# Kernel tuning notes

Hardware: AMD Instinct MI355X
Metric: run time of the kernel (lower is better)

Reference implementation:

```python
import jax, jax.numpy as jnp
import numpy as np

C_IN = 768
CA = 384


def dwconv3d(x, w, b, pad):
    # x: [B, Ca, T, H, W], w: [Ca, 1, kd, kh, kw] depthwise (groups=Ca)
    y = jax.lax.conv_general_dilated(
        x, w, window_strides=(1, 1, 1), padding=pad,
        dimension_numbers=("NCDHW", "OIDHW", "NCDHW"),
        feature_group_count=w.shape[0])
    return y + b[None, :, None, None, None]


def setup_inputs() -> dict:
    key = jax.random.key(0)
    ks = jax.random.split(key, 9)
    s = 0.02
    inp = {
        "x": jax.random.normal(ks[0], (128, 197, C_IN), dtype=jnp.float32),
        # main branch params (torch Linear weight transposed to [in, out])
        "w1": jax.random.normal(ks[1], (C_IN, CA), dtype=jnp.float32) * s,
        "b1": jnp.zeros((CA,), jnp.float32),
        "cw": jax.random.normal(ks[2], (CA, 1, 3, 3, 3), dtype=jnp.float32) * s,
        "cb": jnp.zeros((CA,), jnp.float32),
        "w2": jax.random.normal(ks[3], (CA, C_IN), dtype=jnp.float32) * s,
        "b2": jnp.zeros((C_IN,), jnp.float32),
        # offset-adapter params (depthwise kernel (1,3,3))
        "ow1": jax.random.normal(ks[4], (C_IN, CA), dtype=jnp.float32) * s,
        "ob1": jnp.zeros((CA,), jnp.float32),
        "ocw": jax.random.normal(ks[5], (CA, 1, 1, 3, 3), dtype=jnp.float32) * s,
        "ocb": jnp.zeros((CA,), jnp.float32),
        "ow2": jax.random.normal(ks[6], (CA, C_IN), dtype=jnp.float32) * s,
        "ob2": jnp.zeros((C_IN,), jnp.float32),
        "T": 8,
    }
    return inp


def reference(x, w1, b1, cw, cb, w2, b2, ow1, ob1, ocw, ocb, ow2, ob2, T):
    BT, L, C = x.shape
    B = BT // T
    H = W = int(round((L - 1) ** 0.5))
    Ca = w1.shape[1]

    xs = x[:, 1:, :].reshape(B, T, H * W, C)  # drop CLS token

    # ---- OffsetAdapter branch ----
    x_former = jnp.concatenate([xs[:, :1], xs[:, :-1]], axis=1)  # former_id = [0,0,1,...,T-2]
    off = xs - x_former
    off = off @ ow1 + ob1                                   # [B,T,HW,Ca]
    off = off.reshape(B, T, H, W, Ca).transpose(0, 4, 1, 2, 3)  # [B,Ca,T,H,W]
    off = dwconv3d(off, ocw, ocb, [(0, 0), (1, 1), (1, 1)])
    off = off.transpose(0, 2, 3, 4, 1).reshape(BT, H * W, Ca)
    off = off @ ow2 + ob2                                   # [BT,HW,C]

    # ---- main branch ----
    y = xs @ w1 + b1                                        # [B,T,HW,Ca]
    y = y.reshape(B, T, H, W, Ca).transpose(0, 4, 1, 2, 3)  # [B,Ca,T,H,W]
    y = dwconv3d(y, cw, cb, [(1, 1), (1, 1), (1, 1)])
    y = y.transpose(0, 2, 3, 4, 1).reshape(BT, H * W, Ca)
    y = y @ w2 + b2 + off                                   # [BT,HW,C]

    # residual add into patch tokens (CLS passthrough)
    return x.at[:, 1:, :].add(y)
```

## Files before the change

kernel.cpp:

```cpp
#include <hip/hip_runtime.h>

#define Cc   768
#define CAc  384
#define Bc   16
#define Tc   8
#define Hc   14
#define Wc   14
#define HWc  196
#define Lc   197
#define BTc  128
#define Mc   25088

typedef unsigned short u16;
typedef __attribute__((ext_vector_type(4))) float f32x4;
typedef __attribute__((ext_vector_type(4))) short s16x4;
typedef __attribute__((ext_vector_type(8))) short s16x8;

__device__ __forceinline__ u16 f2b(float f) {
  union { float f; unsigned u; } v; v.f = f;
  unsigned r = (v.u + 0x7FFFu + ((v.u >> 16) & 1u)) >> 16;
  return (u16)r;
}
__device__ __forceinline__ float b2f(u16 h) {
  union { unsigned u; float f; } v; v.u = ((unsigned)h) << 16;
  return v.f;
}

__global__ void wt_kernel(const float* __restrict__ w, u16* __restrict__ wT, int K, int N) {
  int idx = blockIdx.x * 256 + threadIdx.x;
  if (idx >= K * N) return;
  int n = idx / K, k = idx - n * K;
  wT[idx] = f2b(w[k * N + n]);
}

__global__ void cwt_kernel(const float* __restrict__ cw, float* __restrict__ cwT, int taps) {
  int idx = blockIdx.x * 256 + threadIdx.x;
  if (idx >= taps * CAc) return;
  int t = idx / CAc, c = idx - t * CAc;
  cwT[idx] = cw[c * taps + t];
}

__global__ void prep_kernel(const float* __restrict__ x, u16* __restrict__ xb, u16* __restrict__ db) {
  int idx = blockIdx.x * 256 + threadIdx.x;
  if (idx >= Mc * 96) return;
  int r = idx / 96;
  int cg = idx - r * 96;
  int b = r / (Tc * HWc);
  int rem = r - b * (Tc * HWc);
  int t = rem / HWc;
  int hw = rem - t * HWc;
  long xoff = ((long)(b * Tc + t) * Lc + 1 + hw) * Cc + cg * 8;
  long poff = (t > 0) ? (xoff - (long)Lc * Cc) : xoff;
  f32x4 ca = *(const f32x4*)(x + xoff);
  f32x4 cb = *(const f32x4*)(x + xoff + 4);
  f32x4 pa = *(const f32x4*)(x + poff);
  f32x4 pb = *(const f32x4*)(x + poff + 4);
  s16x8 xo, dd;
  #pragma unroll
  for (int q = 0; q < 4; ++q) {
    xo[q]     = (short)f2b(ca[q]);
    xo[q + 4] = (short)f2b(cb[q]);
    dd[q]     = (short)f2b(ca[q] - pa[q]);
    dd[q + 4] = (short)f2b(cb[q] - pb[q]);
  }
  *(s16x8*)(xb + (long)r * Cc + cg * 8) = xo;
  *(s16x8*)(db + (long)r * Cc + cg * 8) = dd;
}

__global__ void cls_kernel(const float* __restrict__ x, float* __restrict__ out) {
  int idx = blockIdx.x * 256 + threadIdx.x;
  if (idx >= BTc * (Cc / 4)) return;
  int bt = idx / (Cc / 4);
  int c4 = (idx - bt * (Cc / 4)) * 4;
  long o = (long)bt * Lc * Cc + c4;
  *(f32x4*)(out + o) = *(const f32x4*)(x + o);
}

#define SP 68

__global__ __launch_bounds__(256, 2) void gemm1_kernel(
    const u16* __restrict__ xb, const u16* __restrict__ db,
    const u16* __restrict__ w1T, const u16* __restrict__ ow1T,
    const float* __restrict__ b1v, const float* __restrict__ ob1v,
    u16* __restrict__ y1, u16* __restrict__ o1)
{
  __shared__ u16 lA[128 * SP];
  __shared__ u16 lB[128 * SP];
  const u16* A    = blockIdx.z ? db   : xb;
  const u16* Wt   = blockIdx.z ? ow1T : w1T;
  const float* bv = blockIdx.z ? ob1v : b1v;
  u16* outp       = blockIdx.z ? o1   : y1;

  int tid = threadIdx.x;
  int m0 = blockIdx.x * 128;
  int n0 = blockIdx.y * 128;
  int wave = tid >> 6, lane = tid & 63;
  int wm = (wave >> 1) * 64, wn = (wave & 1) * 64;
  int lrow = lane & 15, lgrp = lane >> 4;
  int srow = tid >> 3;
  int scol = (tid & 7) * 8;

  f32x4 acc[4][4];
  #pragma unroll
  for (int i = 0; i < 4; ++i)
    #pragma unroll
    for (int j = 0; j < 4; ++j) acc[i][j] = (f32x4){0.f, 0.f, 0.f, 0.f};

  for (int kt = 0; kt < 12; ++kt) {
    int k0 = kt * 64;
    #pragma unroll
    for (int p = 0; p < 4; ++p) {
      int r = p * 32 + srow;
      s16x8 va = *(const s16x8*)(A  + (long)(m0 + r) * Cc + k0 + scol);
      s16x8 vb = *(const s16x8*)(Wt + (long)(n0 + r) * Cc + k0 + scol);
      *(s16x4*)(lA + r * SP + scol)     = ((s16x4*)&va)[0];
      *(s16x4*)(lA + r * SP + scol + 4) = ((s16x4*)&va)[1];
      *(s16x4*)(lB + r * SP + scol)     = ((s16x4*)&vb)[0];
      *(s16x4*)(lB + r * SP + scol + 4) = ((s16x4*)&vb)[1];
    }
    __syncthreads();
    #pragma unroll
    for (int kk = 0; kk < 4; ++kk) {
      s16x4 af[4], bf[4];
      #pragma unroll
      for (int i = 0; i < 4; ++i) af[i] = *(const s16x4*)(lA + (wm + i * 16 + lrow) * SP + kk * 16 + lgrp * 4);
      #pragma unroll
      for (int j = 0; j < 4; ++j) bf[j] = *(const s16x4*)(lB + (wn + j * 16 + lrow) * SP + kk * 16 + lgrp * 4);
      #pragma unroll
      for (int i = 0; i < 4; ++i)
        #pragma unroll
        for (int j = 0; j < 4; ++j)
          acc[i][j] = __builtin_amdgcn_mfma_f32_16x16x16bf16_1k(af[i], bf[j], acc[i][j], 0, 0, 0);
    }
    __syncthreads();
  }
  #pragma unroll
  for (int i = 0; i < 4; ++i) {
    #pragma unroll
    for (int j = 0; j < 4; ++j) {
      int n = n0 + wn + j * 16 + lrow;
      float bb = bv[n];
      #pragma unroll
      for (int q = 0; q < 4; ++q) {
        int m = m0 + wm + i * 16 + lgrp * 4 + q;
        outp[(long)m * CAc + n] = f2b(acc[i][j][q] + bb);
      }
    }
  }
}

__global__ __launch_bounds__(256, 2) void gemm2_kernel(
    const u16* __restrict__ c1, const u16* __restrict__ c2,
    const u16* __restrict__ w2T, const u16* __restrict__ ow2T,
    const float* __restrict__ b2v, const float* __restrict__ ob2v,
    const float* __restrict__ x, float* __restrict__ out)
{
  __shared__ u16 lA[128 * SP];
  __shared__ u16 lB[128 * SP];
  int tid = threadIdx.x;
  int m0 = blockIdx.x * 128;
  int n0 = blockIdx.y * 128;
  int wave = tid >> 6, lane = tid & 63;
  int wm = (wave >> 1) * 64, wn = (wave & 1) * 64;
  int lrow = lane & 15, lgrp = lane >> 4;
  int srow = tid >> 3;
  int scol = (tid & 7) * 8;

  f32x4 acc[4][4];
  #pragma unroll
  for (int i = 0; i < 4; ++i)
    #pragma unroll
    for (int j = 0; j < 4; ++j) acc[i][j] = (f32x4){0.f, 0.f, 0.f, 0.f};

  for (int kt = 0; kt < 12; ++kt) {
    int half = kt >= 6;
    const u16* Ap = half ? c2 : c1;
    const u16* Wp = half ? ow2T : w2T;
    int k0 = (half ? (kt - 6) : kt) * 64;
    #pragma unroll
    for (int p = 0; p < 4; ++p) {
      int r = p * 32 + srow;
      s16x8 va = *(const s16x8*)(Ap + (long)(m0 + r) * CAc + k0 + scol);
      s16x8 vb = *(const s16x8*)(Wp + (long)(n0 + r) * CAc + k0 + scol);
      *(s16x4*)(lA + r * SP + scol)     = ((s16x4*)&va)[0];
      *(s16x4*)(lA + r * SP + scol + 4) = ((s16x4*)&va)[1];
      *(s16x4*)(lB + r * SP + scol)     = ((s16x4*)&vb)[0];
      *(s16x4*)(lB + r * SP + scol + 4) = ((s16x4*)&vb)[1];
    }
    __syncthreads();
    #pragma unroll
    for (int kk = 0; kk < 4; ++kk) {
      s16x4 af[4], bf[4];
      #pragma unroll
      for (int i = 0; i < 4; ++i) af[i] = *(const s16x4*)(lA + (wm + i * 16 + lrow) * SP + kk * 16 + lgrp * 4);
      #pragma unroll
      for (int j = 0; j < 4; ++j) bf[j] = *(const s16x4*)(lB + (wn + j * 16 + lrow) * SP + kk * 16 + lgrp * 4);
      #pragma unroll
      for (int i = 0; i < 4; ++i)
        #pragma unroll
        for (int j = 0; j < 4; ++j)
          acc[i][j] = __builtin_amdgcn_mfma_f32_16x16x16bf16_1k(af[i], bf[j], acc[i][j], 0, 0, 0);
    }
    __syncthreads();
  }
  #pragma unroll
  for (int i = 0; i < 4; ++i) {
    #pragma unroll
    for (int q = 0; q < 4; ++q) {
      int m = m0 + wm + i * 16 + lgrp * 4 + q;
      int bt = m / HWc;
      int hw = m - bt * HWc;
      long base = ((long)bt * Lc + 1 + hw) * Cc;
      #pragma unroll
      for (int j = 0; j < 4; ++j) {
        int n = n0 + wn + j * 16 + lrow;
        out[base + n] = x[base + n] + acc[i][j][q] + b2v[n] + ob2v[n];
      }
    }
  }
}

__global__ void conv_kernel(const u16* __restrict__ in, const float* __restrict__ wT,
                            const float* __restrict__ bias, u16* __restrict__ outp,
                            int is3d)
{
  int bth = blockIdx.x;
  int h = bth % Hc;
  int bt = bth / Hc;
  int t = bt % Tc;
  int tid = threadIdx.x;
  int dtlo = is3d ? -1 : 0, dthi = is3d ? 1 : 0;
  for (int it = tid; it < Wc * 48; it += 256) {
    int wq = it / 48;
    int c = (it - wq * 48) * 8;
    float a[8] = {0.f, 0.f, 0.f, 0.f, 0.f, 0.f, 0.f, 0.f};
    int tap = 0;
    for (int dt = dtlo; dt <= dthi; ++dt) {
      int tt = t + dt;
      bool tok = (tt >= 0) && (tt < Tc);
      for (int dh = -1; dh <= 1; ++dh) {
        int hh = h + dh;
        bool hok = (hh >= 0) && (hh < Hc);
        for (int dw = -1; dw <= 1; ++dw, ++tap) {
          int ww = wq + dw;
          if (!tok || !hok || ww < 0 || ww >= Wc) continue;
          const u16* ip = in + ((long)(bt + dt) * HWc + hh * Wc + ww) * CAc + c;
          s16x8 v = *(const s16x8*)ip;
          const float* wp = wT + tap * CAc + c;
          f32x4 w0 = *(const f32x4*)wp;
          f32x4 w1 = *(const f32x4*)(wp + 4);
          #pragma unroll
          for (int q = 0; q < 4; ++q) {
            a[q]     += b2f((u16)v[q])     * w0[q];
            a[q + 4] += b2f((u16)v[q + 4]) * w1[q];
          }
        }
      }
    }
    s16x8 o;
    #pragma unroll
    for (int q = 0; q < 8; ++q) o[q] = (short)f2b(a[q] + bias[c + q]);
    *(s16x8*)(outp + ((long)bt * HWc + h * Wc + wq) * CAc + c) = o;
  }
}

extern "C" void kernel_launch(void* const* d_in, const int* in_sizes, int n_in,
                              void* d_out, int out_size, void* d_ws, size_t ws_size,
                              hipStream_t stream) {
  const float* x   = (const float*)d_in[0];
  const float* w1  = (const float*)d_in[1];
  const float* b1  = (const float*)d_in[2];
  const float* cw  = (const float*)d_in[3];
  const float* cb  = (const float*)d_in[4];
  const float* w2  = (const float*)d_in[5];
  const float* b2  = (const float*)d_in[6];
  const float* ow1 = (const float*)d_in[7];
  const float* ob1 = (const float*)d_in[8];
  const float* ocw = (const float*)d_in[9];
  const float* ocb = (const float*)d_in[10];
  const float* ow2 = (const float*)d_in[11];
  const float* ob2 = (const float*)d_in[12];
  float* out = (float*)d_out;
  char* ws = (char*)d_ws;

  u16*  w1T  = (u16*) (ws + 0);
  u16*  ow1T = (u16*) (ws + 589824);
  u16*  w2T  = (u16*) (ws + 1179648);
  u16*  ow2T = (u16*) (ws + 1769472);
  float* cwT = (float*)(ws + 2359296);
  float* ocwT= (float*)(ws + 2400768);
  u16*  xb   = (u16*) (ws + 2414592);
  u16*  db   = (u16*) (ws + 40949760);
  u16*  y1   = (u16*) (ws + 79484928);
  u16*  o1   = (u16*) (ws + 98752512);
  u16*  c1   = (u16*) (ws + 2414592);
  u16*  c2   = (u16*) (ws + 2414592 + 19267584);

  wt_kernel<<<1152, 256, 0, stream>>>(w1, w1T, 768, 384);
  wt_kernel<<<1152, 256, 0, stream>>>(ow1, ow1T, 768, 384);
  wt_kernel<<<1152, 256, 0, stream>>>(w2, w2T, 384, 768);
  wt_kernel<<<1152, 256, 0, stream>>>(ow2, ow2T, 384, 768);
  cwt_kernel<<<41, 256, 0, stream>>>(cw, cwT, 27);
  cwt_kernel<<<14, 256, 0, stream>>>(ocw, ocwT, 9);
  prep_kernel<<<9408, 256, 0, stream>>>(x, xb, db);
  cls_kernel<<<96, 256, 0, stream>>>(x, out);
  gemm1_kernel<<<dim3(196, 3, 2), 256, 0, stream>>>(xb, db, w1T, ow1T, b1, ob1, y1, o1);
  conv_kernel<<<1792, 256, 0, stream>>>(y1, cwT, cb, c1, 1);
  conv_kernel<<<1792, 256, 0, stream>>>(o1, ocwT, ocb, c2, 0);
  gemm2_kernel<<<dim3(196, 6, 1), 256, 0, stream>>>(c1, c2, w2T, ow2T, b2, ob2, x, out);
}
```

Before: 372.1 us.

## Use 16x16x32 bf16 MFMA, wider LDS ops, tiled weight transpose, merged launches

Both GEMMs switch from the 16x16x16 bf16 MFMA to the 16x16x32 variant, with 8-element LDS reads and writes and the LDS row pitch changed from 68 to 72. Launch bounds are raised to 4 blocks per CU. Weight transposes now go through a shared-memory tile and are merged into two launches, and the two depthwise convolutions are merged into one launch. This cuts instruction count, LDS traffic and launch overhead, at the cost of more register pressure from the higher occupancy target.

```diff
diff --git a/kernel.cpp b/kernel.cpp
--- a/kernel.cpp
+++ b/kernel.cpp
@@ -2,7 +2,6 @@
 
 #define Cc   768
 #define CAc  384
-#define Bc   16
 #define Tc   8
 #define Hc   14
 #define Wc   14
@@ -26,11 +25,25 @@
   return v.f;
 }
 
-__global__ void wt_kernel(const float* __restrict__ w, u16* __restrict__ wT, int K, int N) {
-  int idx = blockIdx.x * 256 + threadIdx.x;
-  if (idx >= K * N) return;
-  int n = idx / K, k = idx - n * K;
-  wT[idx] = f2b(w[k * N + n]);
+__global__ void wt_kernel(const float* __restrict__ wA, u16* __restrict__ wAT,
+                          const float* __restrict__ wB, u16* __restrict__ wBT,
+                          int K, int N) {
+  __shared__ float t[32][33];
+  const float* w = blockIdx.z ? wB : wA;
+  u16* wT = blockIdx.z ? wBT : wAT;
+  int k0 = blockIdx.x * 32, n0 = blockIdx.y * 32;
+  int tx = threadIdx.x & 31, ty = threadIdx.x >> 5;
+  #pragma unroll
+  for (int p = 0; p < 4; ++p) {
+    int r = ty + p * 8;
+    t[r][tx] = w[(long)(k0 + r) * N + n0 + tx];
+  }
+  __syncthreads();
+  #pragma unroll
+  for (int p = 0; p < 4; ++p) {
+    int r = ty + p * 8;
+    wT[(long)(n0 + r) * K + k0 + tx] = f2b(t[tx][r]);
+  }
 }
 
 __global__ void cwt_kernel(const float* __restrict__ cw, float* __restrict__ cwT, int taps) {
@@ -76,9 +89,9 @@
   *(f32x4*)(out + o) = *(const f32x4*)(x + o);
 }
 
-#define SP 68
-
-__global__ __launch_bounds__(256, 2) void gemm1_kernel(
+#define SP 72
+
+__global__ __launch_bounds__(256, 4) void gemm1_kernel(
     const u16* __restrict__ xb, const u16* __restrict__ db,
     const u16* __restrict__ w1T, const u16* __restrict__ ow1T,
     const float* __restrict__ b1v, const float* __restrict__ ob1v,
@@ -104,7 +117,7 @@
   #pragma unroll
   for (int i = 0; i < 4; ++i)
     #pragma unroll
-    for (int j = 0; j < 4; ++j) acc[i][j] = (f32x4){0.f, 0.f, 0.f, 0.f};
+    for (int j = 0; j < 4; ++j) acc[i][j] = (f32x4){0,0,0,0};
 
   for (int kt = 0; kt < 12; ++kt) {
     int k0 = kt * 64;
@@ -113,24 +126,22 @@
       int r = p * 32 + srow;
       s16x8 va = *(const s16x8*)(A  + (long)(m0 + r) * Cc + k0 + scol);
       s16x8 vb = *(const s16x8*)(Wt + (long)(n0 + r) * Cc + k0 + scol);
-      *(s16x4*)(lA + r * SP + scol)     = ((s16x4*)&va)[0];
-      *(s16x4*)(lA + r * SP + scol + 4) = ((s16x4*)&va)[1];
-      *(s16x4*)(lB + r * SP + scol)     = ((s16x4*)&vb)[0];
-      *(s16x4*)(lB + r * SP + scol + 4) = ((s16x4*)&vb)[1];
+      *(s16x8*)(lA + r * SP + scol) = va;
+      *(s16x8*)(lB + r * SP + scol) = vb;
     }
     __syncthreads();
     #pragma unroll
-    for (int kk = 0; kk < 4; ++kk) {
-      s16x4 af[4], bf[4];
-      #pragma unroll
-      for (int i = 0; i < 4; ++i) af[i] = *(const s16x4*)(lA + (wm + i * 16 + lrow) * SP + kk * 16 + lgrp * 4);
-      #pragma unroll
-      for (int j = 0; j < 4; ++j) bf[j] = *(const s16x4*)(lB + (wn + j * 16 + lrow) * SP + kk * 16 + lgrp * 4);
+    for (int kk = 0; kk < 2; ++kk) {
+      s16x8 af[4], bf[4];
+      #pragma unroll
+      for (int i = 0; i < 4; ++i) af[i] = *(const s16x8*)(lA + (wm + i * 16 + lrow) * SP + kk * 32 + lgrp * 8);
+      #pragma unroll
+      for (int j = 0; j < 4; ++j) bf[j] = *(const s16x8*)(lB + (wn + j * 16 + lrow) * SP + kk * 32 + lgrp * 8);
       #pragma unroll
       for (int i = 0; i < 4; ++i)
         #pragma unroll
         for (int j = 0; j < 4; ++j)
-          acc[i][j] = __builtin_amdgcn_mfma_f32_16x16x16bf16_1k(af[i], bf[j], acc[i][j], 0, 0, 0);
+          acc[i][j] = __builtin_amdgcn_mfma_f32_16x16x32_bf16(af[i], bf[j], acc[i][j], 0, 0, 0);
     }
     __syncthreads();
   }
@@ -149,7 +160,7 @@
   }
 }
 
-__global__ __launch_bounds__(256, 2) void gemm2_kernel(
+__global__ __launch_bounds__(256, 4) void gemm2_kernel(
     const u16* __restrict__ c1, const u16* __restrict__ c2,
     const u16* __restrict__ w2T, const u16* __restrict__ ow2T,
     const float* __restrict__ b2v, const float* __restrict__ ob2v,
@@ -170,7 +181,7 @@
   #pragma unroll
   for (int i = 0; i < 4; ++i)
     #pragma unroll
-    for (int j = 0; j < 4; ++j) acc[i][j] = (f32x4){0.f, 0.f, 0.f, 0.f};
+    for (int j = 0; j < 4; ++j) acc[i][j] = (f32x4){0,0,0,0};
 
   for (int kt = 0; kt < 12; ++kt) {
     int half = kt >= 6;
@@ -182,24 +193,22 @@
       int r = p * 32 + srow;
       s16x8 va = *(const s16x8*)(Ap + (long)(m0 + r) * CAc + k0 + scol);
       s16x8 vb = *(const s16x8*)(Wp + (long)(n0 + r) * CAc + k0 + scol);
-      *(s16x4*)(lA + r * SP + scol)     = ((s16x4*)&va)[0];
-      *(s16x4*)(lA + r * SP + scol + 4) = ((s16x4*)&va)[1];
-      *(s16x4*)(lB + r * SP + scol)     = ((s16x4*)&vb)[0];
-      *(s16x4*)(lB + r * SP + scol + 4) = ((s16x4*)&vb)[1];
+      *(s16x8*)(lA + r * SP + scol) = va;
+      *(s16x8*)(lB + r * SP + scol) = vb;
     }
     __syncthreads();
     #pragma unroll
-    for (int kk = 0; kk < 4; ++kk) {
-      s16x4 af[4], bf[4];
-      #pragma unroll
-      for (int i = 0; i < 4; ++i) af[i] = *(const s16x4*)(lA + (wm + i * 16 + lrow) * SP + kk * 16 + lgrp * 4);
-      #pragma unroll
-      for (int j = 0; j < 4; ++j) bf[j] = *(const s16x4*)(lB + (wn + j * 16 + lrow) * SP + kk * 16 + lgrp * 4);
+    for (int kk = 0; kk < 2; ++kk) {
+      s16x8 af[4], bf[4];
+      #pragma unroll
+      for (int i = 0; i < 4; ++i) af[i] = *(const s16x8*)(lA + (wm + i * 16 + lrow) * SP + kk * 32 + lgrp * 8);
+      #pragma unroll
+      for (int j = 0; j < 4; ++j) bf[j] = *(const s16x8*)(lB + (wn + j * 16 + lrow) * SP + kk * 32 + lgrp * 8);
       #pragma unroll
       for (int i = 0; i < 4; ++i)
         #pragma unroll
         for (int j = 0; j < 4; ++j)
-          acc[i][j] = __builtin_amdgcn_mfma_f32_16x16x16bf16_1k(af[i], bf[j], acc[i][j], 0, 0, 0);
+          acc[i][j] = __builtin_amdgcn_mfma_f32_16x16x32_bf16(af[i], bf[j], acc[i][j], 0, 0, 0);
     }
     __syncthreads();
   }
@@ -220,10 +229,17 @@
   }
 }
 
-__global__ void conv_kernel(const u16* __restrict__ in, const float* __restrict__ wT,
-                            const float* __restrict__ bias, u16* __restrict__ outp,
-                            int is3d)
+__global__ void conv_kernel(const u16* __restrict__ in1, const float* __restrict__ wT1,
+                            const float* __restrict__ bias1, u16* __restrict__ out1,
+                            const u16* __restrict__ in2, const float* __restrict__ wT2,
+                            const float* __restrict__ bias2, u16* __restrict__ out2)
 {
+  int is3d = (blockIdx.y == 0);
+  const u16* in = is3d ? in1 : in2;
+  const float* wT = is3d ? wT1 : wT2;
+  const float* bias = is3d ? bias1 : bias2;
+  u16* outp = is3d ? out1 : out2;
+
   int bth = blockIdx.x;
   int h = bth % Hc;
   int bt = bth / Hc;
@@ -233,7 +249,7 @@
   for (int it = tid; it < Wc * 48; it += 256) {
     int wq = it / 48;
     int c = (it - wq * 48) * 8;
-    float a[8] = {0.f, 0.f, 0.f, 0.f, 0.f, 0.f, 0.f, 0.f};
+    float a[8] = {0,0,0,0,0,0,0,0};
     int tap = 0;
     for (int dt = dtlo; dt <= dthi; ++dt) {
       int tt = t + dt;
@@ -294,18 +310,15 @@
   u16*  y1   = (u16*) (ws + 79484928);
   u16*  o1   = (u16*) (ws + 98752512);
   u16*  c1   = (u16*) (ws + 2414592);
-  u16*  c2   = (u16*) (ws + 2414592 + 19267584);
-
-  wt_kernel<<<1152, 256, 0, stream>>>(w1, w1T, 768, 384);
-  wt_kernel<<<1152, 256, 0, stream>>>(ow1, ow1T, 768, 384);
-  wt_kernel<<<1152, 256, 0, stream>>>(w2, w2T, 384, 768);
-  wt_kernel<<<1152, 256, 0, stream>>>(ow2, ow2T, 384, 768);
+  u16*  c2   = (u16*) (ws + 21682176);
+
+  wt_kernel<<<dim3(24, 12, 2), 256, 0, stream>>>(w1, w1T, ow1, ow1T, 768, 384);
+  wt_kernel<<<dim3(12, 24, 2), 256, 0, stream>>>(w2, w2T, ow2, ow2T, 384, 768);
   cwt_kernel<<<41, 256, 0, stream>>>(cw, cwT, 27);
   cwt_kernel<<<14, 256, 0, stream>>>(ocw, ocwT, 9);
+  cls_kernel<<<96, 256, 0, stream>>>(x, out);
   prep_kernel<<<9408, 256, 0, stream>>>(x, xb, db);
-  cls_kernel<<<96, 256, 0, stream>>>(x, out);
   gemm1_kernel<<<dim3(196, 3, 2), 256, 0, stream>>>(xb, db, w1T, ow1T, b1, ob1, y1, o1);
-  conv_kernel<<<1792, 256, 0, stream>>>(y1, cwT, cb, c1, 1);
-  conv_kernel<<<1792, 256, 0, stream>>>(o1, ocwT, ocb, c2, 0);
-  gemm2_kernel<<<dim3(196, 6, 1), 256, 0, stream>>>(c1, c2, w2T, ow2T, b2, ob2, x, out);
-}
+  conv_kernel<<<dim3(1792, 2), 256, 0, stream>>>(y1, cwT, cb, c1, o1, ocwT, ocb, c2);
+  gemm2_kernel<<<dim3(196, 6), 256, 0, stream>>>(c1, c2, w2T, ow2T, b2, ob2, x, out);
+}
```

Result: faster. 344.2 us (-7.5%).
